# Kernel optimization log

Measured on AMD Instinct MI355X. Metric: run time of the kernel, lower is better.

## Reference

```python
import jax, jax.numpy as jnp
import numpy as np

PI = float(np.pi)
LN_EPS = 1e-5
COS_EPS = 1e-6

D_HIDDEN, N_HEADS, D_HEAD, D_MLP = 1024, 16, 64, 4096
B, T = 4, 2048


def _xavier(key, shape):
    # torch xavier_uniform on 3D tensor: fan_in = shape[1]*shape[2]? torch uses
    # fan_in = shape[1] * receptive_field(shape[2:]), fan_out = shape[0] * rf.
    rf = 1
    for s in shape[2:]:
        rf *= s
    fan_in, fan_out = shape[1] * rf, shape[0] * rf
    bound = float(np.sqrt(6.0 / (fan_in + fan_out)))
    return jax.random.uniform(key, shape, jnp.float32, -bound, bound)


def setup_inputs() -> dict:
    key = jax.random.key(0)
    ks = jax.random.split(key, 10)
    x = jax.random.normal(ks[0], (B, T, D_HIDDEN), jnp.float32)
    W_Q = _xavier(ks[1], (N_HEADS, D_HIDDEN, 1))
    W_K = _xavier(ks[2], (N_HEADS, D_HIDDEN, 1))
    W_V = _xavier(ks[3], (N_HEADS, D_HIDDEN, D_HEAD))
    W_O = _xavier(ks[4], (D_HIDDEN, D_HEAD, N_HEADS))
    ln1_w = jnp.ones((D_HIDDEN,), jnp.float32)
    ln1_b = jnp.zeros((D_HIDDEN,), jnp.float32)
    ln2_w = jnp.ones((D_HIDDEN,), jnp.float32)
    ln2_b = jnp.zeros((D_HIDDEN,), jnp.float32)
    s1 = 1.0 / np.sqrt(D_HIDDEN)
    s2 = 1.0 / np.sqrt(D_MLP)
    W1 = jax.random.uniform(ks[5], (D_HIDDEN, D_MLP), jnp.float32, -s1, s1)
    b1 = jax.random.uniform(ks[6], (D_MLP,), jnp.float32, -s1, s1)
    W2 = jax.random.uniform(ks[7], (D_MLP, D_HIDDEN), jnp.float32, -s2, s2)
    b2 = jax.random.uniform(ks[8], (D_HIDDEN,), jnp.float32, -s2, s2)
    return {"x": x, "W_Q": W_Q, "W_K": W_K, "W_V": W_V, "W_O": W_O,
            "ln1_w": ln1_w, "ln1_b": ln1_b, "ln2_w": ln2_w, "ln2_b": ln2_b,
            "W1": W1, "b1": b1, "W2": W2, "b2": b2}


def _layer_norm(x, w, b):
    mu = jnp.mean(x, axis=-1, keepdims=True)
    var = jnp.mean(jnp.square(x - mu), axis=-1, keepdims=True)
    return (x - mu) * jax.lax.rsqrt(var + LN_EPS) * w + b


def _cos_attention(y, W_Q, W_K, W_V, W_O):
    q = jnp.einsum('btd,idh->btih', y, W_Q)  # (B,T,H,1)
    k = jnp.einsum('btd,idh->btih', y, W_K)  # (B,T,H,1)
    V = jnp.einsum('btd,idh->btih', y, W_V)  # (B,T,H,Dh)
    # use_tanh branch
    q = jnp.tanh(q) * (PI / 4)
    k = jnp.tanh(k) * (PI / 4)
    cos_k, sin_k = jnp.cos(k), jnp.sin(k)
    cos_KV = jnp.cumsum(cos_k * V, axis=1)
    sin_KV = jnp.cumsum(sin_k * V, axis=1)
    cos_Q, sin_Q = jnp.cos(q), jnp.sin(q)
    heads = cos_Q * cos_KV + sin_Q * sin_KV  # (B,T,H,Dh)
    # epsilon branch: normalizing denominator
    cos_K = jnp.cumsum(cos_k, axis=1)
    sin_K = jnp.cumsum(sin_k, axis=1)
    denom = cos_Q * cos_K + sin_Q * sin_K + COS_EPS  # (B,T,H,1)
    heads = heads / denom
    return jnp.einsum('dhi,btih->btd', W_O, heads)


def reference(x, W_Q, W_K, W_V, W_O, ln1_w, ln1_b, ln2_w, ln2_b, W1, b1, W2, b2):
    y = _layer_norm(x, ln1_w, ln1_b)
    x = x + _cos_attention(y, W_Q, W_K, W_V, W_O)
    y = _layer_norm(x, ln2_w, ln2_b)
    mlp = jnp.dot(jax.nn.gelu(jnp.dot(y, W1) + b1), W2) + b2
    return x + mlp
```

## Files before the change

kernel.cpp:

```cpp
#include <hip/hip_runtime.h>
#include <hip/hip_bf16.h>
#include <stdint.h>

typedef unsigned short u16;
typedef __attribute__((ext_vector_type(4))) unsigned int u32x4;
typedef __attribute__((ext_vector_type(8))) __bf16 bfx8;
typedef __attribute__((ext_vector_type(4))) float f32x4;

#define PI_F 3.14159265358979323846f

__device__ __forceinline__ float bf2f(u16 u) {
    unsigned v = ((unsigned)u) << 16; float f; __builtin_memcpy(&f, &v, 4); return f;
}
__device__ __forceinline__ u16 f2bf(float f) {
    unsigned u; __builtin_memcpy(&u, &f, 4);
    unsigned r = (u + 0x7fffu + ((u >> 16) & 1u)) >> 16; return (u16)r;
}

__device__ __forceinline__ void glds16(const u16* g, const u16* l) {
    __builtin_amdgcn_global_load_lds(
        (const __attribute__((address_space(1))) unsigned int*)(unsigned long long)g,
        (__attribute__((address_space(3))) unsigned int*)(unsigned int)(unsigned long long)l,
        16, 0, 0);
}

__global__ __launch_bounds__(256)
void tconv_kernel(const float* __restrict__ in, u16* __restrict__ out,
                  int R, int C, long inBatch, long outBatch)
{
    __shared__ float tile[64][65];
    const int tx = threadIdx.x & 63;
    const int ty = threadIdx.x >> 6;
    const int bc = blockIdx.x * 64;
    const int br = blockIdx.y * 64;
    const float* ip = in + (long)blockIdx.z * inBatch;
    u16* op = out + (long)blockIdx.z * outBatch;

    #pragma unroll
    for (int rr = ty; rr < 64; rr += 4) {
        int r = br + rr, c = bc + tx;
        tile[rr][tx] = (r < R && c < C) ? ip[(long)r * C + c] : 0.f;
    }
    __syncthreads();
    #pragma unroll
    for (int rr = ty; rr < 64; rr += 4) {
        int oc = bc + rr;
        int orr = br + tx;
        if (oc < C && orr < R)
            op[(long)oc * R + orr] = f2bf(tile[tx][rr]);
    }
}

template<bool DO_QK>
__global__ __launch_bounds__(256)
void ln_kernel(const float* __restrict__ X, const float* __restrict__ w,
               const float* __restrict__ b, u16* __restrict__ Ybf,
               const float* __restrict__ WQ, const float* __restrict__ WK,
               float* __restrict__ cqA, float* __restrict__ sqA,
               float* __restrict__ ckA, float* __restrict__ skA)
{
    __shared__ float yrow[1024];
    __shared__ float wsum[4], wsq[4];
    const int row = blockIdx.x;
    const int tid = threadIdx.x;
    const int lane = tid & 63;
    const int wv = tid >> 6;

    const float4 xv = ((const float4*)(X + (long)row * 1024))[tid];
    float s  = xv.x + xv.y + xv.z + xv.w;
    float sq = xv.x*xv.x + xv.y*xv.y + xv.z*xv.z + xv.w*xv.w;
    #pragma unroll
    for (int off = 32; off; off >>= 1) {
        s  += __shfl_down(s, off);
        sq += __shfl_down(sq, off);
    }
    if (lane == 0) { wsum[wv] = s; wsq[wv] = sq; }
    __syncthreads();
    const float ts = wsum[0] + wsum[1] + wsum[2] + wsum[3];
    const float tq = wsq[0] + wsq[1] + wsq[2] + wsq[3];
    const float mean = ts * (1.f / 1024.f);
    const float var  = tq * (1.f / 1024.f) - mean * mean;
    const float rstd = rsqrtf(var + 1e-5f);

    const float4 wv4 = ((const float4*)w)[tid];
    const float4 bv4 = ((const float4*)b)[tid];
    const float y0 = (xv.x - mean) * rstd * wv4.x + bv4.x;
    const float y1 = (xv.y - mean) * rstd * wv4.y + bv4.y;
    const float y2 = (xv.z - mean) * rstd * wv4.z + bv4.z;
    const float y3 = (xv.w - mean) * rstd * wv4.w + bv4.w;

    uint2 p;
    p.x = (unsigned)f2bf(y0) | ((unsigned)f2bf(y1) << 16);
    p.y = (unsigned)f2bf(y2) | ((unsigned)f2bf(y3) << 16);
    ((uint2*)(Ybf + (long)row * 1024))[tid] = p;

    if (DO_QK) {
        yrow[tid*4+0] = y0; yrow[tid*4+1] = y1;
        yrow[tid*4+2] = y2; yrow[tid*4+3] = y3;
        __syncthreads();
        #pragma unroll
        for (int i = 0; i < 4; ++i) {
            const int h = wv * 4 + i;
            const float* wqp = WQ + (long)h * 1024;
            const float* wkp = WK + (long)h * 1024;
            float dq = 0.f, dk = 0.f;
            #pragma unroll
            for (int j = 0; j < 16; ++j) {
                const float yv = yrow[lane + 64*j];
                dq = fmaf(yv, wqp[lane + 64*j], dq);
                dk = fmaf(yv, wkp[lane + 64*j], dk);
            }
            #pragma unroll
            for (int off = 32; off; off >>= 1) {
                dq += __shfl_down(dq, off);
                dk += __shfl_down(dk, off);
            }
            if (lane == 0) {
                const float aq = tanhf(dq) * (PI_F * 0.25f);
                const float ak = tanhf(dk) * (PI_F * 0.25f);
                float sv, cv;
                const long o = (long)h * 8192 + row;
                __sincosf(aq, &sv, &cv); cqA[o] = cv; sqA[o] = sv;
                __sincosf(ak, &sv, &cv); ckA[o] = cv; skA[o] = sv;
            }
        }
    }
}

__global__ __launch_bounds__(64)
void scan_kernel(const u16* __restrict__ V,
                 const float* __restrict__ cqA, const float* __restrict__ sqA,
                 const float* __restrict__ ckA, const float* __restrict__ skA,
                 u16* __restrict__ H)
{
    __shared__ u16 vt[64][64];
    __shared__ float lck[64], lsk[64], lrc[64], lrs[64];
    const int b = blockIdx.x >> 4;
    const int h = blockIdx.x & 15;
    const int lane = threadIdx.x;
    const long rowbase = (long)b * 2048;
    const long colbase = (long)h * 64;
    const long qbase = (long)h * 8192 + rowbase;

    float csum = 0.f, ssum = 0.f;
    float carry_c = 0.f, carry_s = 0.f;

    for (int ch = 0; ch < 32; ++ch) {
        const int t0 = ch * 64;
        __syncthreads();
        #pragma unroll
        for (int i = 0; i < 8; ++i) {
            const int tt = i * 8 + (lane >> 3);
            const int c0 = (lane & 7) * 8;
            *(u32x4*)&vt[tt][c0] =
                *(const u32x4*)(V + (rowbase + t0 + tt) * 1024 + colbase + c0);
        }
        {
            const float ck = ckA[qbase + t0 + lane];
            const float sk = skA[qbase + t0 + lane];
            const float cq = cqA[qbase + t0 + lane];
            const float sq = sqA[qbase + t0 + lane];
            float c = ck, sscan = sk;
            #pragma unroll
            for (int off = 1; off < 64; off <<= 1) {
                const float oc = __shfl_up(c, off);
                const float os = __shfl_up(sscan, off);
                if (lane >= off) { c += oc; sscan += os; }
            }
            const float cK = carry_c + c;
            const float sK = carry_s + sscan;
            carry_c += __shfl(c, 63);
            carry_s += __shfl(sscan, 63);
            const float denom = cq * cK + sq * sK + 1e-6f;
            lck[lane] = ck; lsk[lane] = sk;
            lrc[lane] = cq / denom; lrs[lane] = sq / denom;
        }
        __syncthreads();
        u16* outp = H + (rowbase + t0) * 1024 + colbase + lane;
        #pragma unroll 8
        for (int tt = 0; tt < 64; ++tt) {
            const float v = bf2f(vt[tt][lane]);
            csum = fmaf(lck[tt], v, csum);
            ssum = fmaf(lsk[tt], v, ssum);
            const float hv = lrc[tt] * csum + lrs[tt] * ssum;
            outp[(long)tt * 1024] = f2bf(hv);
        }
    }
}

template<int EPI, int BN>
__global__ __launch_bounds__(512, 2)
void gemm256(const u16* __restrict__ A, const u16* __restrict__ B,
             void* __restrict__ Cout, const float* __restrict__ res,
             const float* __restrict__ bias, int M, int N, int K, int nx)
{
    constexpr int NREP = BN / 64;
    constexpr int GPT  = (BN == 256) ? 4 : 3;
    __shared__ u16 As[4 * 256 * 32];
    __shared__ u16 Bs[4 * BN * 32];

    const int tid  = threadIdx.x;
    const int lane = tid & 63;
    const int wave = tid >> 6;
    const int wr = wave >> 2;
    const int wc = wave & 3;

    const int L = blockIdx.x;
    const int xcd = L & 7;
    const int q = L >> 3;
    const int bx = q % nx;
    const int by = (q / nx) * 8 + xcd;
    const int brow = by * 256;
    const int bcol = bx * BN;

    const int srow = tid >> 2;
    const int cd = tid & 3;
    const int csrc = (cd - (srow >> 1)) & 3;
    const u16* AgB = A + (long)(brow + srow) * K + csrc * 8;
    const u16* BgB = B + (long)(bcol + srow) * K + csrc * 8;
    const long rowK128 = (long)128 * K;

    const int rr = lane & 15;
    const int physc = ((lane >> 4) + (rr >> 1)) & 3;
    const int aro = (wr * 128 + rr) * 64 + physc * 16;
    const int bro = (wc * (BN / 4) + rr) * 64 + physc * 16;

    f32x4 acc[8][NREP];
    #pragma unroll
    for (int m = 0; m < 8; ++m)
        #pragma unroll
        for (int n = 0; n < NREP; ++n) acc[m][n] = (f32x4){0.f, 0.f, 0.f, 0.f};

    const int NT = K >> 5;
    const char* Ab = (const char*)As;
    const char* Bb = (const char*)Bs;

    #pragma unroll
    for (int t = 0; t < 3; ++t) {
        const int kof = t * 32;
        glds16(AgB + kof,            &As[t * 8192 + tid * 8]);
        glds16(AgB + kof + rowK128,  &As[t * 8192 + 4096 + tid * 8]);
        glds16(BgB + kof,            &Bs[t * (BN * 32) + tid * 8]);
        if constexpr (BN == 256)
            glds16(BgB + kof + rowK128, &Bs[t * 8192 + 4096 + tid * 8]);
    }
    if constexpr (GPT == 4) asm volatile("s_waitcnt vmcnt(8)" ::: "memory");
    else                    asm volatile("s_waitcnt vmcnt(6)" ::: "memory");
    __builtin_amdgcn_s_barrier();

    for (int kt = 0; kt < NT; ++kt) {
        const int cur = kt & 3;
        const int pf  = (kt + 3) & 3;
        const int kof = ((kt + 3) < NT) ? (kt + 3) * 32 : 0;
        const char* Abuf = Ab + cur * 16384;
        const char* Bbuf = Bb + cur * (BN * 64);

        bfx8 af[8], bf[NREP];
        #pragma unroll
        for (int m = 0; m < 8; ++m)
            af[m] = *(const bfx8*)(Abuf + aro + m * 1024);
        #pragma unroll
        for (int n = 0; n < NREP / 2; ++n)
            bf[n] = *(const bfx8*)(Bbuf + bro + n * 1024);
        glds16(AgB + kof,           &As[pf * 8192 + tid * 8]);
        glds16(AgB + kof + rowK128, &As[pf * 8192 + 4096 + tid * 8]);
        __builtin_amdgcn_s_barrier();
        asm volatile("s_waitcnt lgkmcnt(0)" ::: "memory");
        __builtin_amdgcn_sched_barrier(0);
        __builtin_amdgcn_s_setprio(1);
        #pragma unroll
        for (int m = 0; m < 8; ++m)
            #pragma unroll
            for (int n = 0; n < NREP / 2; ++n)
                acc[m][n] = __builtin_amdgcn_mfma_f32_16x16x32_bf16(
                    af[m], bf[n], acc[m][n], 0, 0, 0);
        __builtin_amdgcn_s_setprio(0);
        __builtin_amdgcn_sched_barrier(0);
        __builtin_amdgcn_s_barrier();

        #pragma unroll
        for (int n = NREP / 2; n < NREP; ++n)
            bf[n] = *(const bfx8*)(Bbuf + bro + n * 1024);
        glds16(BgB + kof, &Bs[pf * (BN * 32) + tid * 8]);
        if constexpr (BN == 256)
            glds16(BgB + kof + rowK128, &Bs[pf * 8192 + 4096 + tid * 8]);
        __builtin_amdgcn_s_barrier();
        asm volatile("s_waitcnt lgkmcnt(0)" ::: "memory");
        __builtin_amdgcn_sched_barrier(0);
        __builtin_amdgcn_s_setprio(1);
        #pragma unroll
        for (int m = 0; m < 8; ++m)
            #pragma unroll
            for (int n = NREP / 2; n < NREP; ++n)
                acc[m][n] = __builtin_amdgcn_mfma_f32_16x16x32_bf16(
                    af[m], bf[n], acc[m][n], 0, 0, 0);
        __builtin_amdgcn_s_setprio(0);
        __builtin_amdgcn_sched_barrier(0);
        if constexpr (GPT == 4) asm volatile("s_waitcnt vmcnt(8)" ::: "memory");
        else                    asm volatile("s_waitcnt vmcnt(6)" ::: "memory");
        __builtin_amdgcn_s_barrier();
    }

    const int crow0 = brow + wr * 128 + (lane >> 4) * 4;
    const int ccol0 = bcol + wc * (BN / 4) + rr;
    #pragma unroll
    for (int m = 0; m < 8; ++m) {
        #pragma unroll
        for (int n = 0; n < NREP; ++n) {
            const int col = ccol0 + n * 16;
            #pragma unroll
            for (int r = 0; r < 4; ++r) {
                const int row = crow0 + m * 16 + r;
                const long idx = (long)row * N + col;
                const float v = acc[m][n][r];
                if (EPI == 0) {
                    ((u16*)Cout)[idx] = f2bf(v);
                } else if (EPI == 1) {
                    ((float*)Cout)[idx] = v + res[idx];
                } else if (EPI == 2) {
                    const float hh = v + bias[col];
                    const float z = 0.7978845608028654f * (hh + 0.044715f * hh * hh * hh);
                    const float e = __expf(2.f * z);
                    const float th = 1.f - 2.f / (e + 1.f);
                    ((u16*)Cout)[idx] = f2bf(0.5f * hh * (1.f + th));
                } else {
                    ((float*)Cout)[idx] = v + res[idx] + bias[col];
                }
            }
        }
    }
}

extern "C" void kernel_launch(void* const* d_in, const int* in_sizes, int n_in,
                              void* d_out, int out_size, void* d_ws, size_t ws_size,
                              hipStream_t stream)
{
    (void)in_sizes; (void)n_in; (void)out_size; (void)ws_size;
    const float* x    = (const float*)d_in[0];
    const float* WQ   = (const float*)d_in[1];
    const float* WK   = (const float*)d_in[2];
    const float* WV   = (const float*)d_in[3];
    const float* WO   = (const float*)d_in[4];
    const float* ln1w = (const float*)d_in[5];
    const float* ln1b = (const float*)d_in[6];
    const float* ln2w = (const float*)d_in[7];
    const float* ln2b = (const float*)d_in[8];
    const float* W1   = (const float*)d_in[9];
    const float* b1   = (const float*)d_in[10];
    const float* W2   = (const float*)d_in[11];
    const float* b2   = (const float*)d_in[12];
    float* out = (float*)d_out;

    char* ws = (char*)d_ws;
    u16*   Ybf  = (u16*)(ws + 0);
    u16*   Vbf  = (u16*)(ws + 16777216);
    u16*   Hbf  = (u16*)(ws + 33554432);
    float* X2   = (float*)(ws + 50331648);
    u16*   H1   = (u16*)(ws + 83886080);
    u16*   WVT  = (u16*)(ws + 150994944);
    u16*   WOT  = (u16*)(ws + 153092096);
    u16*   W1T  = (u16*)(ws + 155189248);
    u16*   W2T  = (u16*)(ws + 163577856);
    float* CQ   = (float*)(ws + 171966464);
    float* SQ   = (float*)(ws + 172490752);
    float* CK   = (float*)(ws + 173015040);
    float* SK   = (float*)(ws + 173539328);

    tconv_kernel<<<dim3(1, 16, 16), 256, 0, stream>>>(WV, WVT, 1024, 64, 1024L*64, 64L*1024);
    tconv_kernel<<<dim3(1, 1, 1024), 256, 0, stream>>>(WO, WOT, 64, 16, 1024L, 1024L);
    tconv_kernel<<<dim3(64, 16, 1), 256, 0, stream>>>(W1, W1T, 1024, 4096, 0L, 0L);
    tconv_kernel<<<dim3(16, 64, 1), 256, 0, stream>>>(W2, W2T, 4096, 1024, 0L, 0L);

    ln_kernel<true><<<8192, 256, 0, stream>>>(x, ln1w, ln1b, Ybf, WQ, WK, CQ, SQ, CK, SK);

    gemm256<0, 128><<<256, 512, 0, stream>>>(Ybf, WVT, Vbf, nullptr, nullptr, 8192, 1024, 1024, 8);

    scan_kernel<<<64, 64, 0, stream>>>(Vbf, CQ, SQ, CK, SK, Hbf);

    gemm256<1, 128><<<256, 512, 0, stream>>>(Hbf, WOT, X2, x, nullptr, 8192, 1024, 1024, 8);

    ln_kernel<false><<<8192, 256, 0, stream>>>(X2, ln2w, ln2b, Ybf,
                                               nullptr, nullptr, nullptr, nullptr, nullptr, nullptr);

    gemm256<2, 256><<<512, 512, 0, stream>>>(Ybf, W1T, H1, nullptr, b1, 8192, 4096, 1024, 16);

    gemm256<3, 128><<<256, 512, 0, stream>>>(H1, W2T, out, X2, b2, 8192, 1024, 4096, 8);
}
```

Before: 522.7 us.

## Rewrite GEMM as 256x256 tile with BK=64 double buffering

Replaces the 4-stage BK=32 pipelined GEMM (BN 128 or 256) with a single 256x256 tile kernel. It uses K-step 64, a two-buffer LDS scheme, an 8-chunk XOR-style swizzle, and four MFMA phases per K-step that interleave A/B fragment loads. The 1024-wide GEMMs now launch 128 blocks instead of 256, which raises per-block reuse but leaves fewer blocks than the GPU's 256 CUs. The new scheme also waits for vmcnt(0) every iteration, which shortens how far global loads run ahead of compute.

Result: slower. 576.0 us (+10.2%).

```diff
diff --git a/kernel.cpp b/kernel.cpp
--- a/kernel.cpp
+++ b/kernel.cpp
@@ -188,17 +188,14 @@
     }
 }
 
-template<int EPI, int BN>
+template<int EPI>
 __global__ __launch_bounds__(512, 2)
 void gemm256(const u16* __restrict__ A, const u16* __restrict__ B,
              void* __restrict__ Cout, const float* __restrict__ res,
              const float* __restrict__ bias, int M, int N, int K, int nx)
 {
-    constexpr int NREP = BN / 64;
-    constexpr int GPT  = (BN == 256) ? 4 : 3;
-    __shared__ u16 As[4 * 256 * 32];
-    __shared__ u16 Bs[4 * BN * 32];
-
+    __shared__ u16 As[2 * 256 * 64];
+    __shared__ u16 Bs[2 * 256 * 64];
     const int tid  = threadIdx.x;
     const int lane = tid & 63;
     const int wave = tid >> 6;
@@ -207,112 +204,152 @@
 
     const int L = blockIdx.x;
     const int xcd = L & 7;
-    const int q = L >> 3;
-    const int bx = q % nx;
-    const int by = (q / nx) * 8 + xcd;
+    const int qq = L >> 3;
+    const int bx = qq % nx;
+    const int by = (qq / nx) * 8 + xcd;
     const int brow = by * 256;
-    const int bcol = bx * BN;
-
-    const int srow = tid >> 2;
-    const int cd = tid & 3;
-    const int csrc = (cd - (srow >> 1)) & 3;
-    const u16* AgB = A + (long)(brow + srow) * K + csrc * 8;
-    const u16* BgB = B + (long)(bcol + srow) * K + csrc * 8;
-    const long rowK128 = (long)128 * K;
+    const int bcol = bx * 256;
+
+    const int srow8 = tid >> 3;
+    const int chp   = tid & 7;
+    const int clog  = (chp - (srow8 & 7)) & 7;
+    const u16* Ag = A + (long)(brow + srow8) * K + clog * 8;
+    const u16* Bg = B + (long)(bcol + srow8) * K + clog * 8;
+    const long rowK64 = (long)64 * K;
 
     const int rr = lane & 15;
-    const int physc = ((lane >> 4) + (rr >> 1)) & 3;
-    const int aro = (wr * 128 + rr) * 64 + physc * 16;
-    const int bro = (wc * (BN / 4) + rr) * 64 + physc * 16;
-
-    f32x4 acc[8][NREP];
-    #pragma unroll
-    for (int m = 0; m < 8; ++m)
-        #pragma unroll
-        for (int n = 0; n < NREP; ++n) acc[m][n] = (f32x4){0.f, 0.f, 0.f, 0.f};
-
-    const int NT = K >> 5;
-    const char* Ab = (const char*)As;
-    const char* Bb = (const char*)Bs;
-
-    #pragma unroll
-    for (int t = 0; t < 3; ++t) {
-        const int kof = t * 32;
-        glds16(AgB + kof,            &As[t * 8192 + tid * 8]);
-        glds16(AgB + kof + rowK128,  &As[t * 8192 + 4096 + tid * 8]);
-        glds16(BgB + kof,            &Bs[t * (BN * 32) + tid * 8]);
-        if constexpr (BN == 256)
-            glds16(BgB + kof + rowK128, &Bs[t * 8192 + 4096 + tid * 8]);
-    }
-    if constexpr (GPT == 4) asm volatile("s_waitcnt vmcnt(8)" ::: "memory");
-    else                    asm volatile("s_waitcnt vmcnt(6)" ::: "memory");
-    __builtin_amdgcn_s_barrier();
-
-    for (int kt = 0; kt < NT; ++kt) {
-        const int cur = kt & 3;
-        const int pf  = (kt + 3) & 3;
-        const int kof = ((kt + 3) < NT) ? (kt + 3) * 32 : 0;
-        const char* Abuf = Ab + cur * 16384;
-        const char* Bbuf = Bb + cur * (BN * 64);
-
-        bfx8 af[8], bf[NREP];
-        #pragma unroll
-        for (int m = 0; m < 8; ++m)
-            af[m] = *(const bfx8*)(Abuf + aro + m * 1024);
-        #pragma unroll
-        for (int n = 0; n < NREP / 2; ++n)
-            bf[n] = *(const bfx8*)(Bbuf + bro + n * 1024);
-        glds16(AgB + kof,           &As[pf * 8192 + tid * 8]);
-        glds16(AgB + kof + rowK128, &As[pf * 8192 + 4096 + tid * 8]);
-        __builtin_amdgcn_s_barrier();
+    const int kq = lane >> 4;
+    const int lo0 = rr * 128 + ((kq + (rr & 7)) & 7) * 16;
+    const int lo1 = rr * 128 + ((kq + 4 + (rr & 7)) & 7) * 16;
+    const char* Ac = (const char*)As;
+    const char* Bc = (const char*)Bs;
+    const int aoff = wr * 16384;
+    const int boff = (wc >> 1) * 16384 + (wc & 1) * 8192;
+
+    f32x4 acc[8][4];
+    #pragma unroll
+    for (int i = 0; i < 8; ++i)
+        #pragma unroll
+        for (int j = 0; j < 4; ++j) acc[i][j] = (f32x4){0.f, 0.f, 0.f, 0.f};
+
+    const int NT = K >> 6;
+
+    #pragma unroll
+    for (int q4 = 0; q4 < 4; ++q4) {
+        glds16(Ag + (long)q4 * rowK64, &As[q4 * 4096 + tid * 8]);
+        glds16(Bg + (long)q4 * rowK64, &Bs[q4 * 4096 + tid * 8]);
+    }
+    asm volatile("s_waitcnt vmcnt(0)" ::: "memory");
+    asm volatile("s_barrier" ::: "memory");
+
+    for (int t = 0; t < NT; ++t) {
+        const int p  = t & 1;
+        const int pn = p ^ 1;
+        const long kofn = (long)((t + 1 < NT) ? (t + 1) : 0) * 64;
+        const char* Ap = Ac + p * 32768;
+        const char* Bp = Bc + p * 32768;
+
+        bfx8 bA[8], bB0[4], bB1[4];
+
+        #pragma unroll
+        for (int m = 0; m < 4; ++m) {
+            bA[m*2+0] = *(const bfx8*)(Ap + aoff + m * 2048 + lo0);
+            bA[m*2+1] = *(const bfx8*)(Ap + aoff + m * 2048 + lo1);
+        }
+        #pragma unroll
+        for (int n = 0; n < 2; ++n) {
+            bB0[n*2+0] = *(const bfx8*)(Bp + boff + n * 2048 + lo0);
+            bB0[n*2+1] = *(const bfx8*)(Bp + boff + n * 2048 + lo1);
+        }
+        #pragma unroll
+        for (int q4 = 0; q4 < 4; ++q4)
+            glds16(Ag + kofn + (long)q4 * rowK64,
+                   &As[pn * 16384 + q4 * 4096 + tid * 8]);
+        asm volatile("s_barrier" ::: "memory");
         asm volatile("s_waitcnt lgkmcnt(0)" ::: "memory");
         __builtin_amdgcn_sched_barrier(0);
         __builtin_amdgcn_s_setprio(1);
         #pragma unroll
-        for (int m = 0; m < 8; ++m)
-            #pragma unroll
-            for (int n = 0; n < NREP / 2; ++n)
-                acc[m][n] = __builtin_amdgcn_mfma_f32_16x16x32_bf16(
-                    af[m], bf[n], acc[m][n], 0, 0, 0);
+        for (int m = 0; m < 4; ++m)
+            #pragma unroll
+            for (int n = 0; n < 2; ++n) {
+                acc[m][n] = __builtin_amdgcn_mfma_f32_16x16x32_bf16(bA[m*2+0], bB0[n*2+0], acc[m][n], 0, 0, 0);
+                acc[m][n] = __builtin_amdgcn_mfma_f32_16x16x32_bf16(bA[m*2+1], bB0[n*2+1], acc[m][n], 0, 0, 0);
+            }
         __builtin_amdgcn_s_setprio(0);
         __builtin_amdgcn_sched_barrier(0);
-        __builtin_amdgcn_s_barrier();
-
-        #pragma unroll
-        for (int n = NREP / 2; n < NREP; ++n)
-            bf[n] = *(const bfx8*)(Bbuf + bro + n * 1024);
-        glds16(BgB + kof, &Bs[pf * (BN * 32) + tid * 8]);
-        if constexpr (BN == 256)
-            glds16(BgB + kof + rowK128, &Bs[pf * 8192 + 4096 + tid * 8]);
-        __builtin_amdgcn_s_barrier();
+        asm volatile("s_barrier" ::: "memory");
+
+        #pragma unroll
+        for (int n = 0; n < 2; ++n) {
+            bB1[n*2+0] = *(const bfx8*)(Bp + boff + (2 + n) * 2048 + lo0);
+            bB1[n*2+1] = *(const bfx8*)(Bp + boff + (2 + n) * 2048 + lo1);
+        }
+        #pragma unroll
+        for (int q4 = 0; q4 < 4; ++q4)
+            glds16(Bg + kofn + (long)q4 * rowK64,
+                   &Bs[pn * 16384 + q4 * 4096 + tid * 8]);
+        asm volatile("s_barrier" ::: "memory");
         asm volatile("s_waitcnt lgkmcnt(0)" ::: "memory");
         __builtin_amdgcn_sched_barrier(0);
         __builtin_amdgcn_s_setprio(1);
         #pragma unroll
-        for (int m = 0; m < 8; ++m)
-            #pragma unroll
-            for (int n = NREP / 2; n < NREP; ++n)
-                acc[m][n] = __builtin_amdgcn_mfma_f32_16x16x32_bf16(
-                    af[m], bf[n], acc[m][n], 0, 0, 0);
+        for (int m = 0; m < 4; ++m)
+            #pragma unroll
+            for (int n = 0; n < 2; ++n) {
+                acc[m][2+n] = __builtin_amdgcn_mfma_f32_16x16x32_bf16(bA[m*2+0], bB1[n*2+0], acc[m][2+n], 0, 0, 0);
+                acc[m][2+n] = __builtin_amdgcn_mfma_f32_16x16x32_bf16(bA[m*2+1], bB1[n*2+1], acc[m][2+n], 0, 0, 0);
+            }
         __builtin_amdgcn_s_setprio(0);
         __builtin_amdgcn_sched_barrier(0);
-        if constexpr (GPT == 4) asm volatile("s_waitcnt vmcnt(8)" ::: "memory");
-        else                    asm volatile("s_waitcnt vmcnt(6)" ::: "memory");
-        __builtin_amdgcn_s_barrier();
+        asm volatile("s_barrier" ::: "memory");
+
+        #pragma unroll
+        for (int m = 0; m < 4; ++m) {
+            bA[m*2+0] = *(const bfx8*)(Ap + aoff + 8192 + m * 2048 + lo0);
+            bA[m*2+1] = *(const bfx8*)(Ap + aoff + 8192 + m * 2048 + lo1);
+        }
+        asm volatile("s_barrier" ::: "memory");
+        asm volatile("s_waitcnt lgkmcnt(0)" ::: "memory");
+        __builtin_amdgcn_sched_barrier(0);
+        __builtin_amdgcn_s_setprio(1);
+        #pragma unroll
+        for (int m = 0; m < 4; ++m)
+            #pragma unroll
+            for (int n = 0; n < 2; ++n) {
+                acc[4+m][2+n] = __builtin_amdgcn_mfma_f32_16x16x32_bf16(bA[m*2+0], bB1[n*2+0], acc[4+m][2+n], 0, 0, 0);
+                acc[4+m][2+n] = __builtin_amdgcn_mfma_f32_16x16x32_bf16(bA[m*2+1], bB1[n*2+1], acc[4+m][2+n], 0, 0, 0);
+            }
+        __builtin_amdgcn_s_setprio(0);
+        __builtin_amdgcn_sched_barrier(0);
+        asm volatile("s_barrier" ::: "memory");
+
+        __builtin_amdgcn_s_setprio(1);
+        #pragma unroll
+        for (int m = 0; m < 4; ++m)
+            #pragma unroll
+            for (int n = 0; n < 2; ++n) {
+                acc[4+m][n] = __builtin_amdgcn_mfma_f32_16x16x32_bf16(bA[m*2+0], bB0[n*2+0], acc[4+m][n], 0, 0, 0);
+                acc[4+m][n] = __builtin_amdgcn_mfma_f32_16x16x32_bf16(bA[m*2+1], bB0[n*2+1], acc[4+m][n], 0, 0, 0);
+            }
+        __builtin_amdgcn_s_setprio(0);
+        __builtin_amdgcn_sched_barrier(0);
+        asm volatile("s_waitcnt vmcnt(0)" ::: "memory");
+        asm volatile("s_barrier" ::: "memory");
     }
 
     const int crow0 = brow + wr * 128 + (lane >> 4) * 4;
-    const int ccol0 = bcol + wc * (BN / 4) + rr;
-    #pragma unroll
-    for (int m = 0; m < 8; ++m) {
-        #pragma unroll
-        for (int n = 0; n < NREP; ++n) {
-            const int col = ccol0 + n * 16;
+    const int ccol0 = bcol + wc * 64 + rr;
+    #pragma unroll
+    for (int mi = 0; mi < 8; ++mi) {
+        #pragma unroll
+        for (int ni = 0; ni < 4; ++ni) {
+            const int col = ccol0 + ni * 16;
             #pragma unroll
             for (int r = 0; r < 4; ++r) {
-                const int row = crow0 + m * 16 + r;
+                const int row = crow0 + mi * 16 + r;
                 const long idx = (long)row * N + col;
-                const float v = acc[m][n][r];
+                const float v = acc[mi][ni][r];
                 if (EPI == 0) {
                     ((u16*)Cout)[idx] = f2bf(v);
                 } else if (EPI == 1) {
@@ -373,16 +410,16 @@
 
     ln_kernel<true><<<8192, 256, 0, stream>>>(x, ln1w, ln1b, Ybf, WQ, WK, CQ, SQ, CK, SK);
 
-    gemm256<0, 128><<<256, 512, 0, stream>>>(Ybf, WVT, Vbf, nullptr, nullptr, 8192, 1024, 1024, 8);
+    gemm256<0><<<128, 512, 0, stream>>>(Ybf, WVT, Vbf, nullptr, nullptr, 8192, 1024, 1024, 4);
 
     scan_kernel<<<64, 64, 0, stream>>>(Vbf, CQ, SQ, CK, SK, Hbf);
 
-    gemm256<1, 128><<<256, 512, 0, stream>>>(Hbf, WOT, X2, x, nullptr, 8192, 1024, 1024, 8);
+    gemm256<1><<<128, 512, 0, stream>>>(Hbf, WOT, X2, x, nullptr, 8192, 1024, 1024, 4);
 
     ln_kernel<false><<<8192, 256, 0, stream>>>(X2, ln2w, ln2b, Ybf,
                                                nullptr, nullptr, nullptr, nullptr, nullptr, nullptr);
 
-    gemm256<2, 256><<<512, 512, 0, stream>>>(Ybf, W1T, H1, nullptr, b1, 8192, 4096, 1024, 16);
-
-    gemm256<3, 128><<<256, 512, 0, stream>>>(H1, W2T, out, X2, b2, 8192, 1024, 4096, 8);
-}
+    gemm256<2><<<512, 512, 0, stream>>>(Ybf, W1T, H1, nullptr, b1, 8192, 4096, 1024, 16);
+
+    gemm256<3><<<128, 512, 0, stream>>>(H1, W2T, out, X2, b2, 8192, 1024, 4096, 4);
+}
```
